# Kernel tuning notes

Measured on AMD Instinct MI355X. Metric: run time of the kernel, lower is better.

Reference implementation:

```python
import jax, jax.numpy as jnp
import numpy as np

B = 4096
OBS_DIM = 1024
E_OUT = 512
H1 = 2048
H2 = 2048


def setup_inputs() -> dict:
    key = jax.random.key(0)
    ks = jax.random.split(key, 12)
    def kaiming(k, shape, fan_in):
        return jax.random.normal(k, shape, dtype=jnp.float32) * np.float32(np.sqrt(2.0 / fan_in))
    obs = jax.random.normal(ks[0], (B, OBS_DIM), dtype=jnp.float32)
    # lineare: Linear(obs_dim, e_outputs), torch weight shape [out, in]
    We = kaiming(ks[1], (E_OUT, OBS_DIM), OBS_DIM)
    be = jax.random.normal(ks[2], (E_OUT,), dtype=jnp.float32) * 0.01
    # obs_dim attention heads, each Linear(e_outputs, 2), stacked
    attn_W = kaiming(ks[3], (OBS_DIM, E_OUT, 2), E_OUT)
    attn_b = jax.random.normal(ks[4], (OBS_DIM, 2), dtype=jnp.float32) * 0.01
    # v_net: Linear(obs_dim,H1)+tanh, Linear(H1,H2)+[dropout(eval:no-op)]+tanh, Linear(H2,1)
    W1 = kaiming(ks[5], (H1, OBS_DIM), OBS_DIM)
    b1 = jnp.zeros((H1,), dtype=jnp.float32)
    W2 = kaiming(ks[6], (H2, H1), H1)
    b2 = jnp.zeros((H2,), dtype=jnp.float32)
    W3 = kaiming(ks[7], (1, H2), H2)
    b3 = jnp.zeros((1,), dtype=jnp.float32)
    return {"obs": obs, "We": We, "be": be, "attn_W": attn_W, "attn_b": attn_b,
            "W1": W1, "b1": b1, "W2": W2, "b2": b2, "W3": W3, "b3": b3}


def reference(obs, We, be, attn_W, attn_b, W1, b1, W2, b2, W3, b3):
    # e = tanh(lineare(obs)) : [B, E_OUT]
    e = jnp.tanh(obs @ We.T + be)
    # all obs_dim attention heads batched into one contraction: [B, OBS_DIM, 2]
    logits = jnp.einsum('be,oec->boc', e, attn_W) + attn_b
    # softmax over the 2 logits, keep prob of class 1 -> Attention [B, OBS_DIM]
    attention = jax.nn.softmax(logits, axis=-1)[..., 1]
    state_attention = obs * attention
    # v_net (eval mode: dropout is identity)
    h = jnp.tanh(state_attention @ W1.T + b1)
    h = jnp.tanh(h @ W2.T + b2)
    v = jnp.squeeze(h @ W3.T + b3, -1)  # [B]
    return (v, attention)
```

## Files before the change

### kernel.cpp

```cpp
#include <hip/hip_runtime.h>
#include <hip/hip_bf16.h>

typedef unsigned short u16;
typedef u16 u16x4 __attribute__((ext_vector_type(4)));
typedef u16 u16x8 __attribute__((ext_vector_type(8)));
typedef __bf16 bf16x8 __attribute__((ext_vector_type(8)));
typedef float f32x4 __attribute__((ext_vector_type(4)));

__device__ __forceinline__ u16 f2bf(float f) {
  unsigned u = __float_as_uint(f);
  u += 0x7FFFu + ((u >> 16) & 1u);
  return (u16)(u >> 16);
}
__device__ __forceinline__ float bf2f(u16 h) {
  return __uint_as_float(((unsigned)h) << 16);
}
__device__ __forceinline__ float tanh_fast(float x) {
  float t = __expf(2.0f * x);
  return 1.0f - 2.0f / (t + 1.0f);
}
__device__ __forceinline__ float sigmoid_fast(float x) {
  return 1.0f / (1.0f + __expf(-x));
}

__device__ __forceinline__ void cvt4(const float* __restrict__ s, u16* __restrict__ d, int q) {
  float4 v = ((const float4*)s)[q];
  u16x4 o = { f2bf(v.x), f2bf(v.y), f2bf(v.z), f2bf(v.w) };
  ((u16x4*)d)[q] = o;
}

__global__ __launch_bounds__(256)
void prep_kernel(const float* __restrict__ obs, const float* __restrict__ We,
                 const float* __restrict__ W1, const float* __restrict__ W2,
                 const float* __restrict__ aW, const float* __restrict__ ab,
                 u16* __restrict__ obs_b, u16* __restrict__ We_b,
                 u16* __restrict__ W1_b, u16* __restrict__ W2_b,
                 u16* __restrict__ Wd, float* __restrict__ bd,
                 float* __restrict__ vzero) {
  int q = blockIdx.x * 256 + threadIdx.x;
  if (q < 1024) ((float4*)vzero)[q] = (float4){0.f, 0.f, 0.f, 0.f};
  if (q < 1048576) { cvt4(obs, obs_b, q); return; }
  q -= 1048576;
  if (q < 131072) { cvt4(We, We_b, q); return; }
  q -= 131072;
  if (q < 524288) { cvt4(W1, W1_b, q); return; }
  q -= 524288;
  if (q < 1048576) { cvt4(W2, W2_b, q); return; }
  q -= 1048576;
  if (q < 131072) {
    int i0 = q * 4;
    int o = i0 >> 9, e0 = i0 & 511;
    const float* p = aW + (size_t)o * 1024 + e0 * 2;
    float4 v0 = *(const float4*)p;
    float4 v1 = *(const float4*)(p + 4);
    u16x4 od = { f2bf(v0.y - v0.x), f2bf(v0.w - v0.z),
                 f2bf(v1.y - v1.x), f2bf(v1.w - v1.z) };
    *(u16x4*)(Wd + i0) = od;
    if (q < 256) {
      float4 a0 = *(const float4*)(ab + q * 8);
      float4 a1 = *(const float4*)(ab + q * 8 + 4);
      float4 ob = { a0.y - a0.x, a0.w - a0.z, a1.y - a1.x, a1.w - a1.z };
      *(float4*)(bd + q * 4) = ob;
    }
  }
}

template <int BM, int BN, int EP>
__global__ __launch_bounds__(256, 2)
void gemm_bt(const u16* __restrict__ A, const u16* __restrict__ Bt,
             int N, int K,
             const float* __restrict__ bias,
             u16* __restrict__ outb, float* __restrict__ outf,
             const u16* __restrict__ obsb, u16* __restrict__ sa,
             const float* __restrict__ W3, const float* __restrict__ b3,
             float* __restrict__ vout) {
  constexpr int LS = 72;
  constexpr int CA = BM / 32;
  constexpr int CB = BN / 32;
  constexpr int MI = BM / 32;
  constexpr int NJ = BN / 32;

  __shared__ __align__(16) u16 As[BM * LS];
  __shared__ __align__(16) u16 Bs[BN * LS];

  const int tid = threadIdx.x;
  const int lane = tid & 63;
  const int wave = tid >> 6;
  const int bm = blockIdx.x, bn = blockIdx.y;

  const int r0 = tid >> 3;
  const int kc = (tid & 7) * 8;

  const u16* gA[CA];
  const u16* gB[CB];
#pragma unroll
  for (int q = 0; q < CA; ++q)
    gA[q] = A + (size_t)(bm * BM + r0 + q * 32) * K + kc;
#pragma unroll
  for (int q = 0; q < CB; ++q)
    gB[q] = Bt + (size_t)(bn * BN + r0 + q * 32) * K + kc;

  u16x8 pa[CA], pb[CB];
#pragma unroll
  for (int q = 0; q < CA; ++q) { pa[q] = *(const u16x8*)gA[q]; gA[q] += 64; }
#pragma unroll
  for (int q = 0; q < CB; ++q) { pb[q] = *(const u16x8*)gB[q]; gB[q] += 64; }

  const int wm = (wave >> 1) * (BM / 2);
  const int wn = (wave & 1) * (BN / 2);
  const int fr = lane & 15;
  const int koff = (lane >> 4) * 8;

  f32x4 acc[MI][NJ];
#pragma unroll
  for (int i = 0; i < MI; ++i)
#pragma unroll
    for (int j = 0; j < NJ; ++j)
      acc[i][j] = (f32x4){0.f, 0.f, 0.f, 0.f};

  const int T = K >> 6;
  for (int k = 0; k < T; ++k) {
    __syncthreads();
#pragma unroll
    for (int q = 0; q < CA; ++q) *(u16x8*)(As + (r0 + q * 32) * LS + kc) = pa[q];
#pragma unroll
    for (int q = 0; q < CB; ++q) *(u16x8*)(Bs + (r0 + q * 32) * LS + kc) = pb[q];
    __syncthreads();

    if (k + 1 < T) {
#pragma unroll
      for (int q = 0; q < CA; ++q) { pa[q] = *(const u16x8*)gA[q]; gA[q] += 64; }
#pragma unroll
      for (int q = 0; q < CB; ++q) { pb[q] = *(const u16x8*)gB[q]; gB[q] += 64; }
    }

#pragma unroll
    for (int s = 0; s < 2; ++s) {
      bf16x8 a[MI], b[NJ];
#pragma unroll
      for (int i = 0; i < MI; ++i)
        a[i] = *(const bf16x8*)(As + (wm + i * 16 + fr) * LS + s * 32 + koff);
#pragma unroll
      for (int j = 0; j < NJ; ++j)
        b[j] = *(const bf16x8*)(Bs + (wn + j * 16 + fr) * LS + s * 32 + koff);
#pragma unroll
      for (int i = 0; i < MI; ++i)
#pragma unroll
        for (int j = 0; j < NJ; ++j)
          acc[i][j] = __builtin_amdgcn_mfma_f32_16x16x32_bf16(a[i], b[j], acc[i][j], 0, 0, 0);
    }
  }

  if constexpr (EP == 2) {
    float vpart[MI][4];
#pragma unroll
    for (int i = 0; i < MI; ++i)
#pragma unroll
      for (int r = 0; r < 4; ++r) vpart[i][r] = 0.f;
#pragma unroll
    for (int j = 0; j < NJ; ++j) {
      const int col = bn * BN + wn + j * 16 + fr;
      const float bv = bias[col];
      const float w3 = W3[col];
#pragma unroll
      for (int i = 0; i < MI; ++i)
#pragma unroll
        for (int r = 0; r < 4; ++r)
          vpart[i][r] += tanh_fast(acc[i][j][r] + bv) * w3;
    }
    const bool lead = (fr == 0);
    const bool addb = (bn == 0) && ((wave & 1) == 0);
#pragma unroll
    for (int i = 0; i < MI; ++i)
#pragma unroll
      for (int r = 0; r < 4; ++r) {
        float p = vpart[i][r];
        p += __shfl_xor(p, 8);
        p += __shfl_xor(p, 4);
        p += __shfl_xor(p, 2);
        p += __shfl_xor(p, 1);
        if (lead) {
          const int row = bm * BM + wm + i * 16 + (lane >> 4) * 4 + r;
          atomicAdd(vout + row, addb ? p + b3[0] : p);
        }
      }
  } else {
#pragma unroll
    for (int j = 0; j < NJ; ++j) {
      const int col = bn * BN + wn + j * 16 + fr;
      const float bv = bias[col];
#pragma unroll
      for (int i = 0; i < MI; ++i) {
#pragma unroll
        for (int r = 0; r < 4; ++r) {
          const int row = bm * BM + wm + i * 16 + (lane >> 4) * 4 + r;
          const float x = acc[i][j][r] + bv;
          const size_t idx = (size_t)row * N + col;
          if constexpr (EP == 0) {
            outb[idx] = f2bf(tanh_fast(x));
          } else {
            const float att = sigmoid_fast(x);
            outf[idx] = att;
            sa[idx] = f2bf(bf2f(obsb[idx]) * att);
          }
        }
      }
    }
  }
}

extern "C" void kernel_launch(void* const* d_in, const int* in_sizes, int n_in,
                              void* d_out, int out_size, void* d_ws, size_t ws_size,
                              hipStream_t stream) {
  const float* obs   = (const float*)d_in[0];
  const float* We    = (const float*)d_in[1];
  const float* be    = (const float*)d_in[2];
  const float* attnW = (const float*)d_in[3];
  const float* attnb = (const float*)d_in[4];
  const float* W1    = (const float*)d_in[5];
  const float* b1    = (const float*)d_in[6];
  const float* W2    = (const float*)d_in[7];
  const float* b2    = (const float*)d_in[8];
  const float* W3    = (const float*)d_in[9];
  const float* b3    = (const float*)d_in[10];
  float* out = (float*)d_out;

  char* ws = (char*)d_ws;
  u16*   We_b  = (u16*)(ws + 0x00000000);
  u16*   Wd_b  = (u16*)(ws + 0x00100000);
  u16*   W1_b  = (u16*)(ws + 0x00200000);
  u16*   W2_b  = (u16*)(ws + 0x00600000);
  float* bd    = (float*)(ws + 0x00E00000);
  u16*   obs_b = (u16*)(ws + 0x00E01000);
  u16*   e_b   = (u16*)(ws + 0x01601000);
  u16*   sa_b  = (u16*)(ws + 0x01A01000);
  u16*   h1_b  = (u16*)(ws + 0x02201000);

  prep_kernel<<<11264, 256, 0, stream>>>(obs, We, W1, W2, attnW, attnb,
                                         obs_b, We_b, W1_b, W2_b, Wd_b, bd, out);

  gemm_bt<64, 64, 0><<<dim3(64, 8), 256, 0, stream>>>(
      obs_b, We_b, 512, 1024, be, e_b, nullptr, nullptr, nullptr, nullptr, nullptr, nullptr);
  gemm_bt<128, 64, 1><<<dim3(32, 16), 256, 0, stream>>>(
      e_b, Wd_b, 1024, 512, bd, nullptr, out + 4096, obs_b, sa_b, nullptr, nullptr, nullptr);
  gemm_bt<128, 128, 0><<<dim3(32, 16), 256, 0, stream>>>(
      sa_b, W1_b, 2048, 1024, b1, h1_b, nullptr, nullptr, nullptr, nullptr, nullptr, nullptr);
  gemm_bt<128, 128, 2><<<dim3(32, 16), 256, 0, stream>>>(
      h1_b, W2_b, 2048, 2048, b2, nullptr, nullptr, nullptr, nullptr, W3, b3, out);
}
```

Baseline: 205.8 us.

## Load A fragments directly from global into registers, bypassing LDS

The GEMM kernel now reads A-operand MFMA fragments straight from global memory into registers with a two-stage register double buffer, and only stages B through shared memory. This removes the LDS writes and reads for A and halves shared memory use. In exchange, wave pairs sharing rows fetch A twice from cache, and the doubled fragment registers raise VGPR pressure.

```diff
diff --git a/kernel.cpp b/kernel.cpp
--- a/kernel.cpp
+++ b/kernel.cpp
@@ -67,7 +67,7 @@
 
 template <int BM, int BN, int EP>
 __global__ __launch_bounds__(256, 2)
-void gemm_bt(const u16* __restrict__ A, const u16* __restrict__ Bt,
+void gemm_ad(const u16* __restrict__ A, const u16* __restrict__ Bt,
              int N, int K,
              const float* __restrict__ bias,
              u16* __restrict__ outb, float* __restrict__ outf,
@@ -75,12 +75,10 @@
              const float* __restrict__ W3, const float* __restrict__ b3,
              float* __restrict__ vout) {
   constexpr int LS = 72;
-  constexpr int CA = BM / 32;
   constexpr int CB = BN / 32;
   constexpr int MI = BM / 32;
   constexpr int NJ = BN / 32;
 
-  __shared__ __align__(16) u16 As[BM * LS];
   __shared__ __align__(16) u16 Bs[BN * LS];
 
   const int tid = threadIdx.x;
@@ -90,19 +88,12 @@
 
   const int r0 = tid >> 3;
   const int kc = (tid & 7) * 8;
-
-  const u16* gA[CA];
   const u16* gB[CB];
-#pragma unroll
-  for (int q = 0; q < CA; ++q)
-    gA[q] = A + (size_t)(bm * BM + r0 + q * 32) * K + kc;
 #pragma unroll
   for (int q = 0; q < CB; ++q)
     gB[q] = Bt + (size_t)(bn * BN + r0 + q * 32) * K + kc;
 
-  u16x8 pa[CA], pb[CB];
-#pragma unroll
-  for (int q = 0; q < CA; ++q) { pa[q] = *(const u16x8*)gA[q]; gA[q] += 64; }
+  u16x8 pb[CB];
 #pragma unroll
   for (int q = 0; q < CB; ++q) { pb[q] = *(const u16x8*)gB[q]; gB[q] += 64; }
 
@@ -111,6 +102,19 @@
   const int fr = lane & 15;
   const int koff = (lane >> 4) * 8;
 
+  const u16* gA[MI];
+#pragma unroll
+  for (int i = 0; i < MI; ++i)
+    gA[i] = A + (size_t)(bm * BM + wm + i * 16 + fr) * K + koff;
+
+  bf16x8 af0[MI][2], af1[MI][2];
+#pragma unroll
+  for (int i = 0; i < MI; ++i) {
+#pragma unroll
+    for (int s = 0; s < 2; ++s) af0[i][s] = *(const bf16x8*)(gA[i] + s * 32);
+    gA[i] += 64;
+  }
+
   f32x4 acc[MI][NJ];
 #pragma unroll
   for (int i = 0; i < MI; ++i)
@@ -119,27 +123,25 @@
       acc[i][j] = (f32x4){0.f, 0.f, 0.f, 0.f};
 
   const int T = K >> 6;
-  for (int k = 0; k < T; ++k) {
+
+  auto body = [&](bf16x8 (&cur)[MI][2], bf16x8 (&nxt)[MI][2], bool last) {
     __syncthreads();
-#pragma unroll
-    for (int q = 0; q < CA; ++q) *(u16x8*)(As + (r0 + q * 32) * LS + kc) = pa[q];
 #pragma unroll
     for (int q = 0; q < CB; ++q) *(u16x8*)(Bs + (r0 + q * 32) * LS + kc) = pb[q];
     __syncthreads();
-
-    if (k + 1 < T) {
-#pragma unroll
-      for (int q = 0; q < CA; ++q) { pa[q] = *(const u16x8*)gA[q]; gA[q] += 64; }
+    if (!last) {
 #pragma unroll
       for (int q = 0; q < CB; ++q) { pb[q] = *(const u16x8*)gB[q]; gB[q] += 64; }
-    }
-
+#pragma unroll
+      for (int i = 0; i < MI; ++i) {
+#pragma unroll
+        for (int s = 0; s < 2; ++s) nxt[i][s] = *(const bf16x8*)(gA[i] + s * 32);
+        gA[i] += 64;
+      }
+    }
 #pragma unroll
     for (int s = 0; s < 2; ++s) {
-      bf16x8 a[MI], b[NJ];
-#pragma unroll
-      for (int i = 0; i < MI; ++i)
-        a[i] = *(const bf16x8*)(As + (wm + i * 16 + fr) * LS + s * 32 + koff);
+      bf16x8 b[NJ];
 #pragma unroll
       for (int j = 0; j < NJ; ++j)
         b[j] = *(const bf16x8*)(Bs + (wn + j * 16 + fr) * LS + s * 32 + koff);
@@ -147,8 +149,13 @@
       for (int i = 0; i < MI; ++i)
 #pragma unroll
         for (int j = 0; j < NJ; ++j)
-          acc[i][j] = __builtin_amdgcn_mfma_f32_16x16x32_bf16(a[i], b[j], acc[i][j], 0, 0, 0);
-    }
+          acc[i][j] = __builtin_amdgcn_mfma_f32_16x16x32_bf16(cur[i][s], b[j], acc[i][j], 0, 0, 0);
+    }
+  };
+
+  for (int k = 0; k < T; k += 2) {
+    body(af0, af1, false);
+    body(af1, af0, k + 2 >= T);
   }
 
   if constexpr (EP == 2) {
@@ -239,12 +246,12 @@
   prep_kernel<<<11264, 256, 0, stream>>>(obs, We, W1, W2, attnW, attnb,
                                          obs_b, We_b, W1_b, W2_b, Wd_b, bd, out);
 
-  gemm_bt<64, 64, 0><<<dim3(64, 8), 256, 0, stream>>>(
+  gemm_ad<64, 64, 0><<<dim3(64, 8), 256, 0, stream>>>(
       obs_b, We_b, 512, 1024, be, e_b, nullptr, nullptr, nullptr, nullptr, nullptr, nullptr);
-  gemm_bt<128, 64, 1><<<dim3(32, 16), 256, 0, stream>>>(
+  gemm_ad<128, 64, 1><<<dim3(32, 16), 256, 0, stream>>>(
       e_b, Wd_b, 1024, 512, bd, nullptr, out + 4096, obs_b, sa_b, nullptr, nullptr, nullptr);
-  gemm_bt<128, 128, 0><<<dim3(32, 16), 256, 0, stream>>>(
+  gemm_ad<128, 128, 0><<<dim3(32, 16), 256, 0, stream>>>(
       sa_b, W1_b, 2048, 1024, b1, h1_b, nullptr, nullptr, nullptr, nullptr, nullptr, nullptr);
-  gemm_bt<128, 128, 2><<<dim3(32, 16), 256, 0, stream>>>(
+  gemm_ad<128, 128, 2><<<dim3(32, 16), 256, 0, stream>>>(
       h1_b, W2_b, 2048, 2048, b2, nullptr, nullptr, nullptr, nullptr, W3, b3, out);
 }
```

Measured after the change: 271.1 us. +31.7%, slower.

## Use direct global-to-LDS async loads in new 64x128 GEMM kernel for big layers

Applied to the files above, without the earlier changes.

Adds a gemm_g2 kernel for the two large v_net GEMMs. It uses global_load_lds to copy tiles straight from global memory into shared memory, skipping the register staging step. The kernel uses 128-thread blocks with 64x128 tiles, K steps of 32, and an unpadded LDS layout. The aim is to cut register pressure and load-instruction overhead, but with a single buffer and two barriers per small K step there is no prefetch overlap, and the unpadded LDS rows may cause bank conflicts.

```diff
diff --git a/kernel.cpp b/kernel.cpp
--- a/kernel.cpp
+++ b/kernel.cpp
@@ -21,6 +21,12 @@
 }
 __device__ __forceinline__ float sigmoid_fast(float x) {
   return 1.0f / (1.0f + __expf(-x));
+}
+__device__ __forceinline__ void async16(const void* g, void* lds) {
+  __builtin_amdgcn_global_load_lds(
+      (const __attribute__((address_space(1))) unsigned int*)g,
+      (__attribute__((address_space(3))) unsigned int*)lds,
+      16, 0, 0);
 }
 
 __device__ __forceinline__ void cvt4(const float* __restrict__ s, u16* __restrict__ d, int q) {
@@ -71,9 +77,7 @@
              int N, int K,
              const float* __restrict__ bias,
              u16* __restrict__ outb, float* __restrict__ outf,
-             const u16* __restrict__ obsb, u16* __restrict__ sa,
-             const float* __restrict__ W3, const float* __restrict__ b3,
-             float* __restrict__ vout) {
+             const u16* __restrict__ obsb, u16* __restrict__ sa) {
   constexpr int LS = 72;
   constexpr int CA = BM / 32;
   constexpr int CB = BN / 32;
@@ -151,27 +155,114 @@
     }
   }
 
+#pragma unroll
+  for (int j = 0; j < NJ; ++j) {
+    const int col = bn * BN + wn + j * 16 + fr;
+    const float bv = bias[col];
+#pragma unroll
+    for (int i = 0; i < MI; ++i) {
+#pragma unroll
+      for (int r = 0; r < 4; ++r) {
+        const int row = bm * BM + wm + i * 16 + (lane >> 4) * 4 + r;
+        const float x = acc[i][j][r] + bv;
+        const size_t idx = (size_t)row * N + col;
+        if constexpr (EP == 0) {
+          outb[idx] = f2bf(tanh_fast(x));
+        } else {
+          const float att = sigmoid_fast(x);
+          outf[idx] = att;
+          sa[idx] = f2bf(bf2f(obsb[idx]) * att);
+        }
+      }
+    }
+  }
+}
+
+template <int EP>
+__global__ __launch_bounds__(128, 2)
+void gemm_g2(const u16* __restrict__ A, const u16* __restrict__ Bt,
+             int N, int K,
+             const float* __restrict__ bias,
+             u16* __restrict__ outb,
+             const float* __restrict__ W3, const float* __restrict__ b3,
+             float* __restrict__ vout) {
+  __shared__ __align__(16) u16 As[64 * 32];
+  __shared__ __align__(16) u16 Bs[128 * 32];
+
+  const int tid = threadIdx.x;
+  const int lane = tid & 63;
+  const int wave = tid >> 6;
+  const int bm = blockIdx.x, bn = blockIdx.y;
+
+  const u16* gsrc[6];
+  u16* ldst[6];
+#pragma unroll
+  for (int q = 0; q < 6; ++q) {
+    const int c = wave * 6 + q;
+    if (c < 4) {
+      gsrc[q] = A + (size_t)(bm * 64 + c * 16 + (lane >> 2)) * K + (lane & 3) * 8;
+      ldst[q] = As + c * 512;
+    } else {
+      gsrc[q] = Bt + (size_t)(bn * 128 + (c - 4) * 16 + (lane >> 2)) * K + (lane & 3) * 8;
+      ldst[q] = Bs + (c - 4) * 512;
+    }
+  }
+
+  const int wn = wave * 64;
+  const int fr = lane & 15;
+  const int koff = (lane >> 4) * 8;
+
+  f32x4 acc[4][4];
+#pragma unroll
+  for (int i = 0; i < 4; ++i)
+#pragma unroll
+    for (int j = 0; j < 4; ++j)
+      acc[i][j] = (f32x4){0.f, 0.f, 0.f, 0.f};
+
+  const int T = K >> 5;
+  for (int k = 0; k < T; ++k) {
+    __syncthreads();
+#pragma unroll
+    for (int q = 0; q < 6; ++q) async16(gsrc[q], ldst[q]);
+#pragma unroll
+    for (int q = 0; q < 6; ++q) gsrc[q] += 32;
+    __syncthreads();
+
+    bf16x8 a[4], b[4];
+#pragma unroll
+    for (int i = 0; i < 4; ++i)
+      a[i] = *(const bf16x8*)(As + (i * 16 + fr) * 32 + koff);
+#pragma unroll
+    for (int j = 0; j < 4; ++j)
+      b[j] = *(const bf16x8*)(Bs + (wn + j * 16 + fr) * 32 + koff);
+#pragma unroll
+    for (int i = 0; i < 4; ++i)
+#pragma unroll
+      for (int j = 0; j < 4; ++j)
+        acc[i][j] = __builtin_amdgcn_mfma_f32_16x16x32_bf16(a[i], b[j], acc[i][j], 0, 0, 0);
+  }
+
   if constexpr (EP == 2) {
-    float vpart[MI][4];
-#pragma unroll
-    for (int i = 0; i < MI; ++i)
+    float vpart[4][4];
+#pragma unroll
+    for (int i = 0; i < 4; ++i)
 #pragma unroll
       for (int r = 0; r < 4; ++r) vpart[i][r] = 0.f;
 #pragma unroll
-    for (int j = 0; j < NJ; ++j) {
-      const int col = bn * BN + wn + j * 16 + fr;
+    for (int j = 0; j < 4; ++j) {
+      const int col = bn * 128 + wn + j * 16 + fr;
       const float bv = bias[col];
       const float w3 = W3[col];
 #pragma unroll
-      for (int i = 0; i < MI; ++i)
+      for (int i = 0; i < 4; ++i)
 #pragma unroll
         for (int r = 0; r < 4; ++r)
           vpart[i][r] += tanh_fast(acc[i][j][r] + bv) * w3;
     }
     const bool lead = (fr == 0);
-    const bool addb = (bn == 0) && ((wave & 1) == 0);
-#pragma unroll
-    for (int i = 0; i < MI; ++i)
+    const bool addb = (bn == 0) && (wave == 0);
+#pragma unroll
+    for (int i = 0; i < 4; ++i)
 #pragma unroll
       for (int r = 0; r < 4; ++r) {
         float p = vpart[i][r];
@@ -180,29 +271,21 @@
         p += __shfl_xor(p, 2);
         p += __shfl_xor(p, 1);
         if (lead) {
-          const int row = bm * BM + wm + i * 16 + (lane >> 4) * 4 + r;
+          const int row = bm * 64 + i * 16 + (lane >> 4) * 4 + r;
           atomicAdd(vout + row, addb ? p + b3[0] : p);
         }
       }
   } else {
 #pragma unroll
-    for (int j = 0; j < NJ; ++j) {
-      const int col = bn * BN + wn + j * 16 + fr;
+    for (int j = 0; j < 4; ++j) {
+      const int col = bn * 128 + wn + j * 16 + fr;
       const float bv = bias[col];
 #pragma unroll
-      for (int i = 0; i < MI; ++i) {
+      for (int i = 0; i < 4; ++i) {
 #pragma unroll
         for (int r = 0; r < 4; ++r) {
-          const int row = bm * BM + wm + i * 16 + (lane >> 4) * 4 + r;
-          const float x = acc[i][j][r] + bv;
-          const size_t idx = (size_t)row * N + col;
-          if constexpr (EP == 0) {
-            outb[idx] = f2bf(tanh_fast(x));
-          } else {
-            const float att = sigmoid_fast(x);
-            outf[idx] = att;
-            sa[idx] = f2bf(bf2f(obsb[idx]) * att);
-          }
+          const int row = bm * 64 + i * 16 + (lane >> 4) * 4 + r;
+          outb[(size_t)row * N + col] = f2bf(tanh_fast(acc[i][j][r] + bv));
         }
       }
     }
@@ -240,11 +323,11 @@
                                          obs_b, We_b, W1_b, W2_b, Wd_b, bd, out);
 
   gemm_bt<64, 64, 0><<<dim3(64, 8), 256, 0, stream>>>(
-      obs_b, We_b, 512, 1024, be, e_b, nullptr, nullptr, nullptr, nullptr, nullptr, nullptr);
+      obs_b, We_b, 512, 1024, be, e_b, nullptr, nullptr, nullptr);
   gemm_bt<128, 64, 1><<<dim3(32, 16), 256, 0, stream>>>(
-      e_b, Wd_b, 1024, 512, bd, nullptr, out + 4096, obs_b, sa_b, nullptr, nullptr, nullptr);
-  gemm_bt<128, 128, 0><<<dim3(32, 16), 256, 0, stream>>>(
-      sa_b, W1_b, 2048, 1024, b1, h1_b, nullptr, nullptr, nullptr, nullptr, nullptr, nullptr);
-  gemm_bt<128, 128, 2><<<dim3(32, 16), 256, 0, stream>>>(
-      h1_b, W2_b, 2048, 2048, b2, nullptr, nullptr, nullptr, nullptr, W3, b3, out);
-}
+      e_b, Wd_b, 1024, 512, bd, nullptr, out + 4096, obs_b, sa_b);
+  gemm_g2<0><<<dim3(64, 16), 128, 0, stream>>>(
+      sa_b, W1_b, 2048, 1024, b1, h1_b, nullptr, nullptr, nullptr);
+  gemm_g2<2><<<dim3(64, 16), 128, 0, stream>>>(
+      h1_b, W2_b, 2048, 2048, b2, nullptr, W3, b3, out);
+}
```

After: 222.1 us. 7.9% more time.
